# Kernel optimization log

Hardware: AMD Instinct MI355X
Metric: run time of the kernel (lower is better)

## Reference

```python
import jax, jax.numpy as jnp
import numpy as np

EPS_LN = 1e-6   # ln_1 / ln_2 (partial(LayerNorm, eps=1e-6))
EPS_ON = 1e-5   # SS2D out_norm (default LayerNorm eps)


def _ln(x, g, b, eps):
    m = jnp.mean(x, -1, keepdims=True)
    v = jnp.mean(jnp.square(x - m), -1, keepdims=True)
    return (x - m) * jax.lax.rsqrt(v + eps) * g + b


def _dwconv(x, w, b):
    # x: (B,C,H,W), w: (C,1,3,3) depthwise, 'SAME' padding (padding=1 for k=3)
    y = jax.lax.conv_general_dilated(x, w, (1, 1), 'SAME',
        feature_group_count=x.shape[1], dimension_numbers=('NCHW', 'OIHW', 'NCHW'))
    return y + b[None, :, None, None]


def _selective_scan(u, dts, A, Bs, Cs, Ds):
    # u, dts: (B,K,D,L); A: (K,D,N); Bs, Cs: (B,K,N,L); Ds: (K,D)
    B, K, D, L = u.shape
    N = A.shape[-1]
    uT = jnp.moveaxis(u, -1, 0)    # (L,B,K,D)
    dtT = jnp.moveaxis(dts, -1, 0)  # (L,B,K,D)
    BT = jnp.moveaxis(Bs, -1, 0)   # (L,B,K,N)
    CT = jnp.moveaxis(Cs, -1, 0)   # (L,B,K,N)

    def step(h, inp):
        u_t, dt_t, B_t, C_t = inp
        dA = jnp.exp(dt_t[..., None] * A)                                   # (B,K,D,N)
        h = dA * h + (dt_t * u_t)[..., None] * B_t[:, :, None, :]           # (B,K,D,N)
        y = jnp.einsum('bkdn,bkn->bkd', h, C_t)
        return h, y

    h0 = jnp.zeros((B, K, D, N), u.dtype)
    _, ys = jax.lax.scan(step, h0, (uT, dtT, BT, CT))
    ys = jnp.moveaxis(ys, 0, -1)   # (B,K,D,L)
    return ys + u * Ds[None, :, :, None]


def _ss2d(x, in_proj_w, conv_w, conv_b, x_proj_w, dt_w, dt_b, A_logs, Ds,
          onorm_g, onorm_b, out_proj_w):
    # x: (B,H,W,C) -> (B,H,W,C)
    B, H, W, C = x.shape
    Di = in_proj_w.shape[0] // 2
    K = x_proj_w.shape[0]
    R = dt_w.shape[-1]
    N = (x_proj_w.shape[1] - R) // 2
    L = H * W

    xz = x @ in_proj_w.T                       # (B,H,W,2*Di), bias=False
    xx, z = jnp.split(xz, 2, axis=-1)
    xx = jnp.transpose(xx, (0, 3, 1, 2))       # (B,Di,H,W)
    xx = jax.nn.silu(_dwconv(xx, conv_w, conv_b))

    # cross-scan: row-major, col-major, and their reversals
    x0 = xx.reshape(B, Di, L)
    x1 = jnp.transpose(xx, (0, 1, 3, 2)).reshape(B, Di, L)
    xs = jnp.stack([x0, x1, x0[..., ::-1], x1[..., ::-1]], axis=1)  # (B,K,Di,L)

    x_dbl = jnp.einsum('bkdl,kcd->bkcl', xs, x_proj_w)
    dts, Bs, Cs = jnp.split(x_dbl, [R, R + N], axis=2)
    dts = jnp.einsum('bkrl,kdr->bkdl', dts, dt_w)
    dts = jax.nn.softplus(dts + dt_b[None, :, :, None])
    A = -jnp.exp(A_logs.reshape(K, Di, N))

    ys = _selective_scan(xs, dts, A, Bs, Cs, Ds.reshape(K, Di))  # (B,K,Di,L)

    # cross-merge back to row-major
    y0 = ys[:, 0]
    y1 = jnp.transpose(ys[:, 1].reshape(B, Di, W, H), (0, 1, 3, 2)).reshape(B, Di, L)
    y2 = ys[:, 2, :, ::-1]
    y3 = jnp.transpose(ys[:, 3, :, ::-1].reshape(B, Di, W, H), (0, 1, 3, 2)).reshape(B, Di, L)
    y = jnp.transpose(y0 + y1 + y2 + y3, (0, 2, 1))              # (B,L,Di)
    y = _ln(y, onorm_g, onorm_b, EPS_ON).reshape(B, H, W, Di)
    y = y * jax.nn.silu(z)
    return y @ out_proj_w.T                    # bias=False


def setup_inputs() -> dict:
    key = jax.random.key(0)
    ks = jax.random.split(key, 16)
    B, H, W, C = 2, 56, 56, 192
    Di, N, K = 2 * C, 16, 4
    R = int(np.ceil(C / 16))                   # dt_rank = 12
    hid = 4 * C
    g = lambda k, shp, s=0.02: (jax.random.normal(k, shp) * s).astype(jnp.float32)
    return dict(
        x=jax.random.normal(ks[0], (B, H, W, C), jnp.float32),
        cpe1_w=g(ks[1], (C, 1, 3, 3), 0.1), cpe1_b=jnp.zeros((C,), jnp.float32),
        ln1_g=jnp.ones((C,), jnp.float32), ln1_b=jnp.zeros((C,), jnp.float32),
        in_proj_w=g(ks[2], (2 * Di, C)),
        conv_w=g(ks[3], (Di, 1, 3, 3), 0.1), conv_b=jnp.zeros((Di,), jnp.float32),
        x_proj_w=g(ks[4], (K, R + 2 * N, Di)),
        dt_w=g(ks[5], (K, Di, R), 0.1),
        dt_b=jnp.full((K, Di), float(np.log(np.expm1(0.01))), jnp.float32),
        A_logs=jnp.log(jnp.tile(jnp.arange(1, N + 1, dtype=jnp.float32), (K * Di, 1))),
        Ds=jnp.ones((K * Di,), jnp.float32),
        onorm_g=jnp.ones((Di,), jnp.float32), onorm_b=jnp.zeros((Di,), jnp.float32),
        out_proj_w=g(ks[6], (C, Di)),
        cpe2_w=g(ks[7], (C, 1, 3, 3), 0.1), cpe2_b=jnp.zeros((C,), jnp.float32),
        ln2_g=jnp.ones((C,), jnp.float32), ln2_b=jnp.zeros((C,), jnp.float32),
        fc1_w=g(ks[8], (hid, C)), fc1_b=jnp.zeros((hid,), jnp.float32),
        fc2_w=g(ks[9], (C, hid)), fc2_b=jnp.zeros((C,), jnp.float32),
    )


def reference(x, cpe1_w, cpe1_b, ln1_g, ln1_b, in_proj_w, conv_w, conv_b,
              x_proj_w, dt_w, dt_b, A_logs, Ds, onorm_g, onorm_b, out_proj_w,
              cpe2_w, cpe2_b, ln2_g, ln2_b, fc1_w, fc1_b, fc2_w, fc2_b):
    # x: (B,H,W,C)
    x = x + jnp.transpose(_dwconv(jnp.transpose(x, (0, 3, 1, 2)), cpe1_w, cpe1_b), (0, 2, 3, 1))
    x = x + _ss2d(_ln(x, ln1_g, ln1_b, EPS_LN), in_proj_w, conv_w, conv_b,
                  x_proj_w, dt_w, dt_b, A_logs, Ds, onorm_g, onorm_b, out_proj_w)
    x = x + jnp.transpose(_dwconv(jnp.transpose(x, (0, 3, 1, 2)), cpe2_w, cpe2_b), (0, 2, 3, 1))
    h = _ln(x, ln2_g, ln2_b, EPS_LN)
    h = jax.nn.gelu(h @ fc1_w.T + fc1_b, approximate=False)
    x = x + (h @ fc2_w.T + fc2_b)
    return x
```

## Files before the change

### kernel.cpp

```cpp
#include <hip/hip_runtime.h>
#include <math.h>

#define BB 2
#define HHH 56
#define WWW 56
#define CC 192
#define LL 3136
#define DI 384
#define KK 4
#define NN 16
#define RR 12
#define CP 44
#define HIDN 768
#define BL (BB*LL)
#define NCH 98
#define CHL 32

typedef __attribute__((ext_vector_type(8))) short bf16x8;
typedef __attribute__((ext_vector_type(4))) float f32x4;

__device__ __forceinline__ float siluf_(float x){ return x/(1.f+__expf(-x)); }
__device__ __forceinline__ float geluf_(float x){ return 0.5f*x*(1.f+erff(x*0.70710678118654752f)); }
__device__ __forceinline__ unsigned short bf16r_(float x){
  unsigned int u = __float_as_uint(x);
  u += 0x7FFFu + ((u>>16)&1u);
  return (unsigned short)(u>>16);
}
__device__ __forceinline__ float bf2f_(unsigned short u){
  return __uint_as_float(((unsigned int)u)<<16);
}

__global__ void k_cvtw(const float* __restrict__ s0, const float* __restrict__ s1,
                       const float* __restrict__ s2, const float* __restrict__ s3,
                       unsigned short* __restrict__ dst){
  int i = blockIdx.x*256 + threadIdx.x;
  if      (i < 147456) dst[i] = bf16r_(s0[i]);
  else if (i < 221184) dst[i] = bf16r_(s1[i-147456]);
  else if (i < 368640) dst[i] = bf16r_(s2[i-221184]);
  else if (i < 516096) dst[i] = bf16r_(s3[i-368640]);
}

__global__ void k_prepx(const float* __restrict__ xp, unsigned short* __restrict__ wXhi,
                        unsigned short* __restrict__ wXlo){
  int idx = blockIdx.x*256 + threadIdx.x;
  if (idx >= 192*384) return;
  int row = idx / 384, d = idx % 384;
  int k = row / 48, j = row % 48;
  float v = 0.f;
  if (j < 12) v = xp[(k*CP + j)*DI + d];
  else if (j >= 16) v = xp[(k*CP + (j-4))*DI + d];
  unsigned short hi = bf16r_(v);
  wXhi[idx] = hi;
  wXlo[idx] = bf16r_(v - bf2f_(hi));
}

__global__ void k_dwconv_res(const float* __restrict__ in, const float* __restrict__ wgt,
                             const float* __restrict__ bias, float* __restrict__ out) {
  int idx = blockIdx.x*256 + threadIdx.x;
  const int total = BB*HHH*WWW*CC;
  if (idx >= total) return;
  int c = idx % CC;
  int w = (idx / CC) % WWW;
  int h = (idx / (CC*WWW)) % HHH;
  int b = idx / (CC*WWW*HHH);
  float acc = bias[c];
  #pragma unroll
  for (int kh=0; kh<3; kh++){
    int hh = h + kh - 1; if (hh < 0 || hh >= HHH) continue;
    #pragma unroll
    for (int kw=0; kw<3; kw++){
      int ww = w + kw - 1; if (ww < 0 || ww >= WWW) continue;
      acc += in[((b*HHH+hh)*WWW+ww)*CC + c] * wgt[c*9 + kh*3 + kw];
    }
  }
  out[idx] = in[idx] + acc;
}

__global__ void k_ln192(const float* __restrict__ in, const float* __restrict__ g,
                        const float* __restrict__ bta, unsigned short* __restrict__ out, float eps) {
  int row = blockIdx.x*4 + (threadIdx.x>>6);
  int lane = threadIdx.x & 63;
  const float* p = in + (size_t)row*CC;
  float v0=p[lane], v1=p[lane+64], v2=p[lane+128];
  float s = v0+v1+v2, s2 = v0*v0+v1*v1+v2*v2;
  #pragma unroll
  for (int off=1; off<64; off<<=1){ s += __shfl_xor(s,off); s2 += __shfl_xor(s2,off); }
  float m = s*(1.f/192.f);
  float var = s2*(1.f/192.f) - m*m;
  float rstd = rsqrtf(var + eps);
  unsigned short* q = out + (size_t)row*CC;
  q[lane]     = bf16r_((v0-m)*rstd*g[lane]     + bta[lane]);
  q[lane+64]  = bf16r_((v1-m)*rstd*g[lane+64]  + bta[lane+64]);
  q[lane+128] = bf16r_((v2-m)*rstd*g[lane+128] + bta[lane+128]);
}

enum { EPI_NONE=0, EPI_RES=1, EPI_BIAS_GELU=2, EPI_BIAS_RES=3 };

template<int MT, int EPI, int OUTBF>
__global__ __launch_bounds__(256) void k_gemm_mfma(const unsigned short* __restrict__ A,
      const unsigned short* __restrict__ W, const float* __restrict__ bias,
      const float* __restrict__ res, void* __restrict__ outp, int M, int Nn, int Kk) {
  __shared__ unsigned short As[MT][40];
  __shared__ unsigned short Bs[64][40];
  constexpr int NI = (MT==128) ? 4 : 2;
  int tid = threadIdx.x;
  int m0 = blockIdx.y*MT, n0 = blockIdx.x*64;
  int wid = tid>>6, lane = tid&63;
  int wm = (MT==128) ? wid*32 : (wid&1)*32;
  int wn = (MT==128) ? 0 : (wid>>1)*32;
  int fr = lane&15, fk = (lane>>4)*8;
  f32x4 acc[2][NI];
  #pragma unroll
  for (int i=0;i<2;i++)
    #pragma unroll
    for (int j=0;j<NI;j++) acc[i][j] = (f32x4){0.f,0.f,0.f,0.f};
  int arow, ak;
  if (MT==128){ arow = tid>>1; ak = (tid&1)*16; }
  else        { arow = tid>>2; ak = (tid&3)*8;  }
  int wrow = tid>>2, wk = (tid&3)*8;
  const unsigned short* Ap = A + (size_t)(m0+arow)*Kk + ak;
  const unsigned short* Wp = W + (size_t)(n0+wrow)*Kk + wk;
  for (int k0=0; k0<Kk; k0+=32){
    __syncthreads();
    if (MT==128){
      uint4 av0 = *(const uint4*)(Ap + k0);
      uint4 av1 = *(const uint4*)(Ap + k0 + 8);
      *(uint4*)&As[arow][ak]   = av0;
      *(uint4*)&As[arow][ak+8] = av1;
    } else {
      *(uint4*)&As[arow][ak] = *(const uint4*)(Ap + k0);
    }
    *(uint4*)&Bs[wrow][wk] = *(const uint4*)(Wp + k0);
    __syncthreads();
    bf16x8 af[2], bfr[NI];
    #pragma unroll
    for (int mi=0;mi<2;mi++) af[mi] = *(const bf16x8*)&As[wm + mi*16 + fr][fk];
    #pragma unroll
    for (int ni=0;ni<NI;ni++) bfr[ni] = *(const bf16x8*)&Bs[wn + ni*16 + fr][fk];
    #pragma unroll
    for (int mi=0;mi<2;mi++)
      #pragma unroll
      for (int ni=0;ni<NI;ni++)
        acc[mi][ni] = __builtin_amdgcn_mfma_f32_16x16x32_bf16(af[mi], bfr[ni], acc[mi][ni], 0,0,0);
  }
  int rbase = (lane>>4)*4;
  #pragma unroll
  for (int mi=0;mi<2;mi++){
    #pragma unroll
    for (int ni=0;ni<NI;ni++){
      int col = n0 + wn + ni*16 + fr;
      float bv = (EPI==EPI_BIAS_GELU || EPI==EPI_BIAS_RES) ? bias[col] : 0.f;
      #pragma unroll
      for (int r=0;r<4;r++){
        int row = m0 + wm + mi*16 + rbase + r;
        float v = acc[mi][ni][r] + bv;
        if (EPI==EPI_BIAS_GELU) v = geluf_(v);
        if (EPI==EPI_RES || EPI==EPI_BIAS_RES) v += res[(size_t)row*Nn + col];
        if (OUTBF) ((unsigned short*)outp)[(size_t)row*Nn + col] = bf16r_(v);
        else       ((float*)outp)[(size_t)row*Nn + col] = v;
      }
    }
  }
}

__global__ __launch_bounds__(256) void k_xgemm(const float* __restrict__ uf,
      const unsigned short* __restrict__ wXhi, const unsigned short* __restrict__ wXlo,
      float* __restrict__ xdblT) {
  __shared__ unsigned short Ah[64][40];
  __shared__ unsigned short Al[64][40];
  __shared__ unsigned short Bh[64][40];
  __shared__ unsigned short Bl[64][40];
  int tid = threadIdx.x;
  int m0 = blockIdx.y*64, n0 = blockIdx.x*64;
  int wid = tid>>6, lane = tid&63;
  int fr = lane&15, fk = (lane>>4)*8;
  f32x4 acc[4];
  #pragma unroll
  for (int j=0;j<4;j++) acc[j] = (f32x4){0.f,0.f,0.f,0.f};
  int srow = tid>>2, sk = (tid&3)*8;
  const float* Ap = uf + (size_t)(m0+srow)*DI + sk;
  const unsigned short* Wh = wXhi + (size_t)(n0+srow)*DI + sk;
  const unsigned short* Wl = wXlo + (size_t)(n0+srow)*DI + sk;
  for (int k0=0; k0<DI; k0+=32){
    __syncthreads();
    float4 ua = *(const float4*)(Ap + k0);
    float4 ub = *(const float4*)(Ap + k0 + 4);
    uint4 wh = *(const uint4*)(Wh + k0);
    uint4 wl = *(const uint4*)(Wl + k0);
    float uv[8] = {ua.x,ua.y,ua.z,ua.w, ub.x,ub.y,ub.z,ub.w};
    #pragma unroll
    for (int j=0;j<8;j++){
      unsigned short hi = bf16r_(uv[j]);
      Ah[srow][sk+j] = hi;
      Al[srow][sk+j] = bf16r_(uv[j] - bf2f_(hi));
    }
    *(uint4*)&Bh[srow][sk] = wh;
    *(uint4*)&Bl[srow][sk] = wl;
    __syncthreads();
    bf16x8 ah = *(const bf16x8*)&Ah[wid*16 + fr][fk];
    bf16x8 al = *(const bf16x8*)&Al[wid*16 + fr][fk];
    #pragma unroll
    for (int ni=0;ni<4;ni++){
      bf16x8 bh = *(const bf16x8*)&Bh[ni*16 + fr][fk];
      bf16x8 bl = *(const bf16x8*)&Bl[ni*16 + fr][fk];
      acc[ni] = __builtin_amdgcn_mfma_f32_16x16x32_bf16(ah, bh, acc[ni], 0,0,0);
      acc[ni] = __builtin_amdgcn_mfma_f32_16x16x32_bf16(al, bh, acc[ni], 0,0,0);
      acc[ni] = __builtin_amdgcn_mfma_f32_16x16x32_bf16(ah, bl, acc[ni], 0,0,0);
    }
  }
  int rbase = (lane>>4)*4;
  #pragma unroll
  for (int ni=0;ni<4;ni++){
    int col = n0 + ni*16 + fr;
    int k = col / 48, j = col % 48;
    #pragma unroll
    for (int r=0;r<4;r++){
      int row = m0 + wid*16 + rbase + r;
      int b = row / LL, s = row % LL;
      int h = s / WWW, w2 = s % WWW;
      int l1 = w2*HHH + h;
      int lk = (k==0) ? s : (k==1) ? l1 : (k==2) ? (LL-1-s) : (LL-1-l1);
      xdblT[((size_t)((b*KK+k)*LL + lk))*48 + j] = acc[ni][r];
    }
  }
}

__global__ void k_conv_xx(const float* __restrict__ xz, const float* __restrict__ cw,
                          const float* __restrict__ cb, float* __restrict__ xc0,
                          float* __restrict__ xc1) {
  int idx = blockIdx.x*256 + threadIdx.x;
  if (idx >= BB*LL*DI) return;
  int d = idx % DI;
  int l = (idx / DI) % LL;
  int b = idx / (DI*LL);
  int h = l / WWW, w = l % WWW;
  float acc = cb[d];
  #pragma unroll
  for (int kh=0; kh<3; kh++){
    int hh = h + kh - 1; if (hh < 0 || hh >= HHH) continue;
    #pragma unroll
    for (int kw=0; kw<3; kw++){
      int ww2 = w + kw - 1; if (ww2 < 0 || ww2 >= WWW) continue;
      acc += xz[((size_t)(b*LL + hh*WWW + ww2))*(2*DI) + d] * cw[d*9 + kh*3 + kw];
    }
  }
  float v = siluf_(acc);
  xc0[idx] = v;
  xc1[((size_t)(b*LL + w*HHH + h))*DI + d] = v;
}

template<int PASS>
__global__ __launch_bounds__(64) void k_scan(const float* __restrict__ xc_l0,
        const float* __restrict__ xc_l1,
        const float* __restrict__ xdblT, const float* __restrict__ dtw, const float* __restrict__ dtb,
        const float* __restrict__ alogs, const float* __restrict__ Dsv,
        unsigned short* __restrict__ hend, float* __restrict__ sumdt, unsigned short* __restrict__ ysb) {
  int ch = blockIdx.y, bk = blockIdx.z;
  int b = bk >> 2, k = bk & 3;
  int d = blockIdx.x*64 + threadIdx.x;
  int kd = k*DI + d;
  float w[12];
  #pragma unroll
  for (int r=0;r<12;r++) w[r] = dtw[kd*12 + r];
  float biasd = dtb[kd];
  float Dd = (PASS==1) ? Dsv[kd] : 0.f;
  float An2[16];
  #pragma unroll
  for (int n=0;n<16;n++) An2[n] = -__expf(alogs[kd*16 + n]) * 1.44269504f;
  bool pw = true;
  #pragma unroll
  for (int n=1;n<16;n++) pw = pw && (fabsf(An2[n] - (float)(n+1)*An2[0]) <= 1e-3f*(float)(n+1)*fabsf(An2[0]));
  const float* usrc = (k & 1) ? xc_l1 : xc_l0;
  bool rev = (k >= 2);
  const float* rec0 = xdblT + ((size_t)bk*LL + ch*CHL)*48;
  float h[16];
  size_t hb = ((size_t)(bk*NCH + ch)*DI + d)*16;
  if (PASS==0){
    #pragma unroll
    for (int n=0;n<16;n++) h[n]=0.f;
  } else {
    uint4 q0 = *(const uint4*)&hend[hb];
    uint4 q1 = *(const uint4*)&hend[hb+8];
    unsigned int qa[8] = {q0.x,q0.y,q0.z,q0.w, q1.x,q1.y,q1.z,q1.w};
    #pragma unroll
    for (int j=0;j<8;j++){
      h[2*j]   = bf2f_((unsigned short)(qa[j] & 0xffffu));
      h[2*j+1] = bf2f_((unsigned short)(qa[j] >> 16));
    }
  }
  float cum = 0.f;
  #pragma unroll 2
  for (int i=0;i<CHL;i++){
    int li = ch*CHL + i;
    int lsrc = rev ? (LL-1-li) : li;
    float uu = usrc[((size_t)(b*LL + lsrc))*DI + d];
    const float* rec = rec0 + (size_t)i*48;
    float4 t0 = *(const float4*)(rec);
    float4 t1 = *(const float4*)(rec+4);
    float4 t2 = *(const float4*)(rec+8);
    float4 B0 = *(const float4*)(rec+16);
    float4 B1 = *(const float4*)(rec+20);
    float4 B2 = *(const float4*)(rec+24);
    float4 B3 = *(const float4*)(rec+28);
    float a0 = fmaf(t0.x,w[0], fmaf(t0.y,w[1], fmaf(t0.z,w[2], t0.w*w[3])));
    float a1 = fmaf(t1.x,w[4], fmaf(t1.y,w[5], fmaf(t1.z,w[6], t1.w*w[7])));
    float a2 = fmaf(t2.x,w[8], fmaf(t2.y,w[9], fmaf(t2.z,w[10], t2.w*w[11])));
    float a = biasd + a0 + (a1 + a2);
    float dt = 0.69314718f * log2f(1.f + exp2f(a*1.44269504f));
    float dtu = dt*uu;
    if (PASS==0) cum += dt;
    float dA[16];
    if (pw){
      float r1 = exp2f(dt*An2[0]);
      float r2 = r1*r1;
      float r3 = r2*r1;
      float r4 = r2*r2;
      float r8 = r4*r4;
      dA[0]=r1;     dA[1]=r2;     dA[2]=r3;     dA[3]=r4;
      dA[4]=r4*r1;  dA[5]=r4*r2;  dA[6]=r4*r3;  dA[7]=r8;
      dA[8]=r8*r1;  dA[9]=r8*r2;  dA[10]=r8*r3; dA[11]=r8*r4;
      dA[12]=r8*dA[4]; dA[13]=r8*dA[5]; dA[14]=r8*dA[6]; dA[15]=r8*r8;
    } else {
      #pragma unroll
      for (int n=0;n<16;n++) dA[n] = exp2f(dt*An2[n]);
    }
    float Bv[16] = {B0.x,B0.y,B0.z,B0.w, B1.x,B1.y,B1.z,B1.w,
                    B2.x,B2.y,B2.z,B2.w, B3.x,B3.y,B3.z,B3.w};
    #pragma unroll
    for (int n=0;n<16;n++) h[n] = fmaf(dA[n], h[n], dtu*Bv[n]);
    if (PASS==1){
      float4 C0 = *(const float4*)(rec+32);
      float4 C1 = *(const float4*)(rec+36);
      float4 C2 = *(const float4*)(rec+40);
      float4 C3 = *(const float4*)(rec+44);
      float y0 = fmaf(h[0], C0.x, fmaf(h[1], C0.y, fmaf(h[2], C0.z, h[3]*C0.w)));
      float y1 = fmaf(h[4], C1.x, fmaf(h[5], C1.y, fmaf(h[6], C1.z, h[7]*C1.w)));
      float y2 = fmaf(h[8], C2.x, fmaf(h[9], C2.y, fmaf(h[10],C2.z, h[11]*C2.w)));
      float y3 = fmaf(h[12],C3.x, fmaf(h[13],C3.y, fmaf(h[14],C3.z, h[15]*C3.w)));
      float y = fmaf(uu, Dd, (y0+y1)+(y2+y3));
      ysb[((size_t)(bk*LL + li))*DI + d] = bf16r_(y);
    }
  }
  if (PASS==0){
    unsigned int pk[8];
    #pragma unroll
    for (int j=0;j<8;j++)
      pk[j] = ((unsigned int)bf16r_(h[2*j+1])<<16) | (unsigned int)bf16r_(h[2*j]);
    *(uint4*)&hend[hb]   = make_uint4(pk[0],pk[1],pk[2],pk[3]);
    *(uint4*)&hend[hb+8] = make_uint4(pk[4],pk[5],pk[6],pk[7]);
    sumdt[(bk*NCH + ch)*DI + d] = cum;
  }
}

__global__ __launch_bounds__(64) void k_scanmid(const float* __restrict__ alogs,
        const float* __restrict__ sumdt, unsigned short* __restrict__ hend) {
  int bid = blockIdx.x;
  int dblk = bid % 96;
  int k = (bid/96) % KK;
  int b = bid/(96*KK);
  int lane = threadIdx.x;
  int d4 = lane>>4, n = lane&15;
  int d = dblk*4 + d4;
  int bk = b*KK + k;
  float Ac2 = -__expf(alogs[(k*DI+d)*16 + n]) * 1.44269504f;
  float H = 0.f;
  for (int c=0;c<NCH;c++){
    float sdt = sumdt[(bk*NCH + c)*DI + d];
    float aexp = exp2f(Ac2 * sdt);
    size_t idx = ((size_t)(bk*NCH + c)*DI + dblk*4)*16 + lane;
    float tmp = bf2f_(hend[idx]);
    hend[idx] = bf16r_(H);
    H = fmaf(aexp, H, tmp);
  }
}

__global__ __launch_bounds__(384) void k_fuse(const unsigned short* __restrict__ ysb,
      const float* __restrict__ xz, const float* __restrict__ og, const float* __restrict__ ob,
      unsigned short* __restrict__ a2) {
  __shared__ float sa[6], sb[6];
  int b = blockIdx.x / LL, l = blockIdx.x % LL;
  int d = threadIdx.x;
  int h_ = l / WWW, w_ = l % WWW;
  int l1 = w_*HHH + h_;
  float y = bf2f_(ysb[((size_t)((b*KK+0)*LL + l))*DI + d])
          + bf2f_(ysb[((size_t)((b*KK+1)*LL + l1))*DI + d])
          + bf2f_(ysb[((size_t)((b*KK+2)*LL + (LL-1-l)))*DI + d])
          + bf2f_(ysb[((size_t)((b*KK+3)*LL + (LL-1-l1)))*DI + d]);
  float s = y, s2 = y*y;
  #pragma unroll
  for (int off=1; off<64; off<<=1){ s += __shfl_xor(s,off); s2 += __shfl_xor(s2,off); }
  int wid = d >> 6;
  if ((d & 63) == 0){ sa[wid] = s; sb[wid] = s2; }
  __syncthreads();
  s = sa[0]+sa[1]+sa[2]+sa[3]+sa[4]+sa[5];
  s2 = sb[0]+sb[1]+sb[2]+sb[3]+sb[4]+sb[5];
  float m = s*(1.f/DI);
  float var = s2*(1.f/DI) - m*m;
  float rstd = rsqrtf(var + 1e-5f);
  float v = (y - m)*rstd*og[d] + ob[d];
  float z = xz[((size_t)(b*LL + l))*(2*DI) + DI + d];
  a2[((size_t)(b*LL + l))*DI + d] = bf16r_(v * siluf_(z));
}

extern "C" void kernel_launch(void* const* d_in, const int* in_sizes, int n_in,
                              void* d_out, int out_size, void* d_ws, size_t ws_size,
                              hipStream_t stream) {
  (void)in_sizes; (void)n_in; (void)out_size; (void)ws_size;
  const float* x       = (const float*)d_in[0];
  const float* cpe1_w  = (const float*)d_in[1];
  const float* cpe1_b  = (const float*)d_in[2];
  const float* ln1_g   = (const float*)d_in[3];
  const float* ln1_b   = (const float*)d_in[4];
  const float* in_proj = (const float*)d_in[5];
  const float* conv_w  = (const float*)d_in[6];
  const float* conv_b  = (const float*)d_in[7];
  const float* x_proj  = (const float*)d_in[8];
  const float* dt_w    = (const float*)d_in[9];
  const float* dt_b    = (const float*)d_in[10];
  const float* A_logs  = (const float*)d_in[11];
  const float* Dsv     = (const float*)d_in[12];
  const float* onorm_g = (const float*)d_in[13];
  const float* onorm_b = (const float*)d_in[14];
  const float* out_proj= (const float*)d_in[15];
  const float* cpe2_w  = (const float*)d_in[16];
  const float* cpe2_b  = (const float*)d_in[17];
  const float* ln2_g   = (const float*)d_in[18];
  const float* ln2_b   = (const float*)d_in[19];
  const float* fc1_w   = (const float*)d_in[20];
  const float* fc1_b   = (const float*)d_in[21];
  const float* fc2_w   = (const float*)d_in[22];
  const float* fc2_b   = (const float*)d_in[23];
  float* out = (float*)d_out;
  float* wsf = (float*)d_ws;

  float* x1    = wsf;
  float* xlnf  = x1 + 1204224;
  float* xz    = xlnf + 1204224;
  float* xc_l0 = xz + 4816896;
  float* xc_l1 = xc_l0 + 2408448;
  float* ysbf  = xc_l1 + 2408448;
  float* hendf = ysbf + 4816896;
  float* sumdt = hendf + 2408448;
  float* xdblT = sumdt + 301056;
  unsigned short* wbf = (unsigned short*)(xdblT + 1204224);
  unsigned short* wXhi = wbf + 516096;
  unsigned short* wXlo = wXhi + 73728;
  unsigned short* xln  = (unsigned short*)xlnf;
  unsigned short* xln2 = (unsigned short*)xlnf;
  unsigned short* ysb  = (unsigned short*)ysbf;
  unsigned short* hend = (unsigned short*)hendf;
  unsigned short* a2   = (unsigned short*)xdblT;
  float* x2   = xc_l0;
  float* x3   = xz;
  unsigned short* hbuf = (unsigned short*)ysbf;
  unsigned short* wIn  = wbf;
  unsigned short* wOut = wbf + 147456;
  unsigned short* wF1  = wbf + 221184;
  unsigned short* wF2  = wbf + 368640;

  k_cvtw<<<2016, 256, 0, stream>>>(in_proj, out_proj, fc1_w, fc2_w, wbf);
  k_prepx<<<288, 256, 0, stream>>>(x_proj, wXhi, wXlo);
  k_dwconv_res<<<(BB*HHH*WWW*CC+255)/256, 256, 0, stream>>>(x, cpe1_w, cpe1_b, x1);
  k_ln192<<<BL/4, 256, 0, stream>>>(x1, ln1_g, ln1_b, xln, 1e-6f);
  k_gemm_mfma<128,EPI_NONE,0><<<dim3(768/64, BL/128), 256, 0, stream>>>(xln, wIn, nullptr, nullptr, xz, BL, 2*DI, CC);
  k_conv_xx<<<(BB*LL*DI+255)/256, 256, 0, stream>>>(xz, conv_w, conv_b, xc_l0, xc_l1);
  k_xgemm<<<dim3(3, BL/64), 256, 0, stream>>>(xc_l0, wXhi, wXlo, xdblT);
  k_scan<0><<<dim3(6, NCH, BB*KK), 64, 0, stream>>>(xc_l0, xc_l1, xdblT, dt_w, dt_b, A_logs, Dsv, hend, sumdt, ysb);
  k_scanmid<<<BB*KK*96, 64, 0, stream>>>(A_logs, sumdt, hend);
  k_scan<1><<<dim3(6, NCH, BB*KK), 64, 0, stream>>>(xc_l0, xc_l1, xdblT, dt_w, dt_b, A_logs, Dsv, hend, sumdt, ysb);
  k_fuse<<<BB*LL, 384, 0, stream>>>(ysb, xz, onorm_g, onorm_b, a2);
  k_gemm_mfma<64,EPI_RES,0><<<dim3(192/64, BL/64), 256, 0, stream>>>(a2, wOut, nullptr, x1, x2, BL, CC, DI);
  k_dwconv_res<<<(BB*HHH*WWW*CC+255)/256, 256, 0, stream>>>(x2, cpe2_w, cpe2_b, x3);
  k_ln192<<<BL/4, 256, 0, stream>>>(x3, ln2_g, ln2_b, xln2, 1e-6f);
  k_gemm_mfma<128,EPI_BIAS_GELU,1><<<dim3(768/64, BL/128), 256, 0, stream>>>(xln2, wF1, fc1_b, nullptr, hbuf, BL, HIDN, CC);
  k_gemm_mfma<64,EPI_BIAS_RES,0><<<dim3(192/64, BL/64), 256, 0, stream>>>(hbuf, wF2, fc2_b, x3, out, BL, CC, HIDN);
}
```

Baseline: 243.0 us.

## Stage scan chunk records in LDS and double-buffer u loads in groups of 8

The scan kernel now copies the chunk's 32x48 projection records (dt, B, C) into shared memory once per block, instead of every thread reading them from global memory each step. The 32-step loop is fully unrolled into four groups of 8, and the u values for the next group are prefetched into registers while the current group is computed, so global load latency overlaps the serial recurrence. The cost is higher register pressure from the unrolling and the two 8-element buffers, plus a block barrier.

```diff
diff --git a/kernel.cpp b/kernel.cpp
--- a/kernel.cpp
+++ b/kernel.cpp
@@ -249,16 +249,95 @@
   xc1[((size_t)(b*LL + w*HHH + h))*DI + d] = v;
 }
 
+
+#define LOADU(arr, g_) do { \
+  _Pragma("unroll") \
+  for (int q_=0;q_<8;q_++){ \
+    int li_ = ch*CHL + (g_)*8 + q_; \
+    int lsrc_ = rev ? (LL-1-li_) : li_; \
+    arr[q_] = usrc[((size_t)(b*LL + lsrc_))*DI + d]; \
+  } \
+} while(0)
+
+#define GRP(g_, arr) do { \
+  _Pragma("unroll") \
+  for (int q_=0;q_<8;q_++){ \
+    int i_ = (g_)*8 + q_; \
+    float uu = arr[q_]; \
+    const float* rec = recs + i_*48; \
+    float4 t0 = *(const float4*)(rec); \
+    float4 t1 = *(const float4*)(rec+4); \
+    float4 t2 = *(const float4*)(rec+8); \
+    float4 B0 = *(const float4*)(rec+16); \
+    float4 B1 = *(const float4*)(rec+20); \
+    float4 B2 = *(const float4*)(rec+24); \
+    float4 B3 = *(const float4*)(rec+28); \
+    float a0 = fmaf(t0.x,w[0], fmaf(t0.y,w[1], fmaf(t0.z,w[2], t0.w*w[3]))); \
+    float a1 = fmaf(t1.x,w[4], fmaf(t1.y,w[5], fmaf(t1.z,w[6], t1.w*w[7]))); \
+    float a2 = fmaf(t2.x,w[8], fmaf(t2.y,w[9], fmaf(t2.z,w[10], t2.w*w[11]))); \
+    float a = biasd + a0 + (a1 + a2); \
+    float dt = 0.69314718f * log2f(1.f + exp2f(a*1.44269504f)); \
+    float dtu = dt*uu; \
+    if (PASS==0) cum += dt; \
+    float dA[16]; \
+    if (pw){ \
+      float r1 = exp2f(dt*An2[0]); \
+      float r2 = r1*r1; float r3 = r2*r1; float r4 = r2*r2; float r8 = r4*r4; \
+      dA[0]=r1;  dA[1]=r2;  dA[2]=r3;  dA[3]=r4; \
+      dA[4]=r4*r1;  dA[5]=r4*r2;  dA[6]=r4*r3;  dA[7]=r8; \
+      dA[8]=r8*r1;  dA[9]=r8*r2;  dA[10]=r8*r3; dA[11]=r8*r4; \
+      dA[12]=r8*r4*r1; dA[13]=r8*r4*r2; dA[14]=r8*r4*r3; dA[15]=r8*r8; \
+    } else { \
+      _Pragma("unroll") \
+      for (int n_=0;n_<16;n_++) dA[n_] = exp2f(dt*An2[n_]); \
+    } \
+    h[0]  = fmaf(dA[0],  h[0],  dtu*B0.x); \
+    h[1]  = fmaf(dA[1],  h[1],  dtu*B0.y); \
+    h[2]  = fmaf(dA[2],  h[2],  dtu*B0.z); \
+    h[3]  = fmaf(dA[3],  h[3],  dtu*B0.w); \
+    h[4]  = fmaf(dA[4],  h[4],  dtu*B1.x); \
+    h[5]  = fmaf(dA[5],  h[5],  dtu*B1.y); \
+    h[6]  = fmaf(dA[6],  h[6],  dtu*B1.z); \
+    h[7]  = fmaf(dA[7],  h[7],  dtu*B1.w); \
+    h[8]  = fmaf(dA[8],  h[8],  dtu*B2.x); \
+    h[9]  = fmaf(dA[9],  h[9],  dtu*B2.y); \
+    h[10] = fmaf(dA[10], h[10], dtu*B2.z); \
+    h[11] = fmaf(dA[11], h[11], dtu*B2.w); \
+    h[12] = fmaf(dA[12], h[12], dtu*B3.x); \
+    h[13] = fmaf(dA[13], h[13], dtu*B3.y); \
+    h[14] = fmaf(dA[14], h[14], dtu*B3.z); \
+    h[15] = fmaf(dA[15], h[15], dtu*B3.w); \
+    if (PASS==1){ \
+      float4 C0 = *(const float4*)(rec+32); \
+      float4 C1 = *(const float4*)(rec+36); \
+      float4 C2 = *(const float4*)(rec+40); \
+      float4 C3 = *(const float4*)(rec+44); \
+      float y0 = fmaf(h[0], C0.x, fmaf(h[1], C0.y, fmaf(h[2], C0.z, h[3]*C0.w))); \
+      float y1 = fmaf(h[4], C1.x, fmaf(h[5], C1.y, fmaf(h[6], C1.z, h[7]*C1.w))); \
+      float y2 = fmaf(h[8], C2.x, fmaf(h[9], C2.y, fmaf(h[10],C2.z, h[11]*C2.w))); \
+      float y3 = fmaf(h[12],C3.x, fmaf(h[13],C3.y, fmaf(h[14],C3.z, h[15]*C3.w))); \
+      float y = fmaf(uu, Dd, (y0+y1)+(y2+y3)); \
+      ysb[((size_t)(bk*LL + ch*CHL + i_))*DI + d] = bf16r_(y); \
+    } \
+  } \
+} while(0)
+
 template<int PASS>
 __global__ __launch_bounds__(64) void k_scan(const float* __restrict__ xc_l0,
         const float* __restrict__ xc_l1,
         const float* __restrict__ xdblT, const float* __restrict__ dtw, const float* __restrict__ dtb,
         const float* __restrict__ alogs, const float* __restrict__ Dsv,
         unsigned short* __restrict__ hend, float* __restrict__ sumdt, unsigned short* __restrict__ ysb) {
+  __shared__ float recs[CHL*48];
   int ch = blockIdx.y, bk = blockIdx.z;
   int b = bk >> 2, k = bk & 3;
-  int d = blockIdx.x*64 + threadIdx.x;
+  int lane = threadIdx.x;
+  int d = blockIdx.x*64 + lane;
   int kd = k*DI + d;
+  const float4* rg = (const float4*)(xdblT + ((size_t)bk*LL + ch*CHL)*48);
+  float4* rs = (float4*)recs;
+  #pragma unroll
+  for (int j=0;j<6;j++) rs[lane + j*64] = rg[lane + j*64];
   float w[12];
   #pragma unroll
   for (int r=0;r<12;r++) w[r] = dtw[kd*12 + r];
@@ -272,7 +351,6 @@
   for (int n=1;n<16;n++) pw = pw && (fabsf(An2[n] - (float)(n+1)*An2[0]) <= 1e-3f*(float)(n+1)*fabsf(An2[0]));
   const float* usrc = (k & 1) ? xc_l1 : xc_l0;
   bool rev = (k >= 2);
-  const float* rec0 = xdblT + ((size_t)bk*LL + ch*CHL)*48;
   float h[16];
   size_t hb = ((size_t)(bk*NCH + ch)*DI + d)*16;
   if (PASS==0){
@@ -288,59 +366,17 @@
       h[2*j+1] = bf2f_((unsigned short)(qa[j] >> 16));
     }
   }
+  float u0[8], u1[8];
   float cum = 0.f;
-  #pragma unroll 2
-  for (int i=0;i<CHL;i++){
-    int li = ch*CHL + i;
-    int lsrc = rev ? (LL-1-li) : li;
-    float uu = usrc[((size_t)(b*LL + lsrc))*DI + d];
-    const float* rec = rec0 + (size_t)i*48;
-    float4 t0 = *(const float4*)(rec);
-    float4 t1 = *(const float4*)(rec+4);
-    float4 t2 = *(const float4*)(rec+8);
-    float4 B0 = *(const float4*)(rec+16);
-    float4 B1 = *(const float4*)(rec+20);
-    float4 B2 = *(const float4*)(rec+24);
-    float4 B3 = *(const float4*)(rec+28);
-    float a0 = fmaf(t0.x,w[0], fmaf(t0.y,w[1], fmaf(t0.z,w[2], t0.w*w[3])));
-    float a1 = fmaf(t1.x,w[4], fmaf(t1.y,w[5], fmaf(t1.z,w[6], t1.w*w[7])));
-    float a2 = fmaf(t2.x,w[8], fmaf(t2.y,w[9], fmaf(t2.z,w[10], t2.w*w[11])));
-    float a = biasd + a0 + (a1 + a2);
-    float dt = 0.69314718f * log2f(1.f + exp2f(a*1.44269504f));
-    float dtu = dt*uu;
-    if (PASS==0) cum += dt;
-    float dA[16];
-    if (pw){
-      float r1 = exp2f(dt*An2[0]);
-      float r2 = r1*r1;
-      float r3 = r2*r1;
-      float r4 = r2*r2;
-      float r8 = r4*r4;
-      dA[0]=r1;     dA[1]=r2;     dA[2]=r3;     dA[3]=r4;
-      dA[4]=r4*r1;  dA[5]=r4*r2;  dA[6]=r4*r3;  dA[7]=r8;
-      dA[8]=r8*r1;  dA[9]=r8*r2;  dA[10]=r8*r3; dA[11]=r8*r4;
-      dA[12]=r8*dA[4]; dA[13]=r8*dA[5]; dA[14]=r8*dA[6]; dA[15]=r8*r8;
-    } else {
-      #pragma unroll
-      for (int n=0;n<16;n++) dA[n] = exp2f(dt*An2[n]);
-    }
-    float Bv[16] = {B0.x,B0.y,B0.z,B0.w, B1.x,B1.y,B1.z,B1.w,
-                    B2.x,B2.y,B2.z,B2.w, B3.x,B3.y,B3.z,B3.w};
-    #pragma unroll
-    for (int n=0;n<16;n++) h[n] = fmaf(dA[n], h[n], dtu*Bv[n]);
-    if (PASS==1){
-      float4 C0 = *(const float4*)(rec+32);
-      float4 C1 = *(const float4*)(rec+36);
-      float4 C2 = *(const float4*)(rec+40);
-      float4 C3 = *(const float4*)(rec+44);
-      float y0 = fmaf(h[0], C0.x, fmaf(h[1], C0.y, fmaf(h[2], C0.z, h[3]*C0.w)));
-      float y1 = fmaf(h[4], C1.x, fmaf(h[5], C1.y, fmaf(h[6], C1.z, h[7]*C1.w)));
-      float y2 = fmaf(h[8], C2.x, fmaf(h[9], C2.y, fmaf(h[10],C2.z, h[11]*C2.w)));
-      float y3 = fmaf(h[12],C3.x, fmaf(h[13],C3.y, fmaf(h[14],C3.z, h[15]*C3.w)));
-      float y = fmaf(uu, Dd, (y0+y1)+(y2+y3));
-      ysb[((size_t)(bk*LL + li))*DI + d] = bf16r_(y);
-    }
-  }
+  LOADU(u0, 0);
+  __syncthreads();
+  LOADU(u1, 1);
+  GRP(0, u0);
+  LOADU(u0, 2);
+  GRP(1, u1);
+  LOADU(u1, 3);
+  GRP(2, u0);
+  GRP(3, u1);
   if (PASS==0){
     unsigned int pk[8];
     #pragma unroll
```

Measured after the change: 649.0 us. +167.1%, slower.
